# Performance work log

Measured on AMD Instinct MI355X. Metric: run time of the kernel, lower is better.

## Reference

```python
import jax, jax.numpy as jnp
import numpy as np

FEAT_DIM, HIDDEN_DIM, ATTN_DIM = 512, 512, 256
B, N = 32, 4096


def setup_inputs() -> dict:
    key = jax.random.key(0)
    ks = jax.random.split(key, 8)
    s_f = 1.0 / np.sqrt(FEAT_DIM)
    s_h = 1.0 / np.sqrt(HIDDEN_DIM)
    s_a = 1.0 / np.sqrt(ATTN_DIM)
    return {
        "feats": jax.random.normal(ks[0], (B, N, FEAT_DIM), jnp.float32),
        "hidden": jax.random.normal(ks[1], (B, HIDDEN_DIM), jnp.float32),
        "Wf": jax.random.uniform(ks[2], (FEAT_DIM, ATTN_DIM), jnp.float32, -s_f, s_f),
        "bf": jax.random.uniform(ks[3], (ATTN_DIM,), jnp.float32, -s_f, s_f),
        "Wh": jax.random.uniform(ks[4], (HIDDEN_DIM, ATTN_DIM), jnp.float32, -s_h, s_h),
        "bh": jax.random.uniform(ks[5], (ATTN_DIM,), jnp.float32, -s_h, s_h),
        "Ws": jax.random.uniform(ks[6], (ATTN_DIM,), jnp.float32, -s_a, s_a),
        "bs": jax.random.uniform(ks[7], (), jnp.float32, -s_a, s_a),
    }


def reference(feats, hidden, Wf, bf, Wh, bh, Ws, bs):
    # f: (B, N, A); h: (B, 1, A)
    f = jnp.einsum("bnd,da->bna", feats, Wf) + bf
    h = (hidden @ Wh + bh)[:, None, :]
    e = jnp.tanh(f + h)
    scores = jnp.einsum("bna,a->bn", e, Ws) + bs  # (B, N)
    alpha = jax.nn.softmax(scores, axis=1)
    ctx = jnp.einsum("bnd,bn->bd", feats, alpha)  # (B, D)
    return (ctx, alpha)
```

## Files before the change

kernel.cpp:

```cpp
#include <hip/hip_runtime.h>

typedef __attribute__((ext_vector_type(8))) short short8;
typedef __attribute__((ext_vector_type(4))) float f32x4;

#define WFT_OFF 0
#define HB_OFF  262144
#define SC_OFF  294912
#define ST_OFF  819200
#define CP_OFF  835584

#define SMEM_MAIN 76032

__device__ __forceinline__ unsigned short f2bf(float f) {
    unsigned u = __builtin_bit_cast(unsigned, f);
    u += 0x7fffu + ((u >> 16) & 1u);
    return (unsigned short)(u >> 16);
}
__device__ __forceinline__ float bf2f(unsigned short h) {
    unsigned u = ((unsigned)h) << 16;
    return __builtin_bit_cast(float, u);
}
__device__ __forceinline__ float fast_tanh(float x) {
    float e2 = __expf(2.0f * x);
    return 1.0f - 2.0f / (e2 + 1.0f);
}
__device__ __forceinline__ void lds_barrier() {
    asm volatile("s_waitcnt lgkmcnt(0)" ::: "memory");
    __builtin_amdgcn_s_barrier();
}

__global__ void wft_kernel(const float* __restrict__ Wf, unsigned short* __restrict__ WfT) {
    __shared__ unsigned short tl[64 * 80];
    const int t = threadIdx.x;
    const int tk = blockIdx.x >> 2, ta = blockIdx.x & 3;
    const int d0 = tk * 64, a0 = ta * 64;
#pragma unroll
    for (int i = 0; i < 16; ++i) {
        int flat = t + 256 * i;
        int dl = flat >> 6, al = flat & 63;
        tl[al * 80 + dl] = f2bf(Wf[(d0 + dl) * 256 + a0 + al]);
    }
    __syncthreads();
#pragma unroll
    for (int i = 0; i < 2; ++i) {
        int u = t + 256 * i;
        int al = u >> 3, q = u & 7;
        *(uint4*)(&WfT[(size_t)(a0 + al) * 512 + d0 + q * 8]) =
            *(const uint4*)(&tl[al * 80 + q * 8]);
    }
}

__global__ void hb_kernel(const float* __restrict__ hidden, const float* __restrict__ Wh,
                          const float* __restrict__ bh, const float* __restrict__ bfv,
                          float* __restrict__ hb) {
    const int b = blockIdx.x, a = threadIdx.x;
    float acc = bh[a] + bfv[a];
    const float* hrow = hidden + b * 512;
#pragma unroll 8
    for (int d = 0; d < 512; ++d)
        acc += hrow[d] * Wh[d * 256 + a];
    hb[b * 256 + a] = acc;
}

__launch_bounds__(512, 4)
__global__ void main_kernel(const float* __restrict__ feats,
                            const unsigned short* __restrict__ WfT,
                            const float* __restrict__ hbg,
                            const float* __restrict__ Ws,
                            float* __restrict__ scores,
                            float* __restrict__ stats,
                            float* __restrict__ ctxp) {
    extern __shared__ char smem[];
    char* Ab       = smem;
    float* scratch = (float*)(smem + 65536);
    float* wpart   = (float*)(smem + 73728);
    float* wbuf    = (float*)(smem + 75776);

    const int t = threadIdx.x;
    const int tile = blockIdx.x;
    const int b = tile >> 6;
    const int row0 = tile * 64;
    const int lane = t & 63, w = t >> 6;
    const int lr = lane & 15, lg = lane >> 4;
    const int sw = (lr & 7) << 4;

    {
        const int ar = t >> 3;
        const int c8 = t & 7;
        const float4* fr = (const float4*)(feats + (size_t)(row0 + ar) * 512);
        char* arow = Ab + ar * 1024;
        const int rsw = (ar & 7) << 4;
#pragma unroll
        for (int i = 0; i < 16; ++i) {
            int f4 = c8 + i * 8;
            float4 v = fr[f4];
            uint2 u;
            u.x = (unsigned)f2bf(v.x) | ((unsigned)f2bf(v.y) << 16);
            u.y = (unsigned)f2bf(v.z) | ((unsigned)f2bf(v.w) << 16);
            *(uint2*)(arow + ((f4 * 8) ^ rsw)) = u;
        }
    }

    float hbv[2], wsv[2];
#pragma unroll
    for (int j = 0; j < 2; ++j) {
        int col = w * 32 + j * 16 + lr;
        hbv[j] = hbg[b * 256 + col];
        wsv[j] = Ws[col];
    }

    lds_barrier();

    f32x4 acc[4][2] = {};
    const unsigned short* bp0 = WfT + (size_t)(w * 32 + lr) * 512 + lg * 8;
    const unsigned short* bp1 = WfT + (size_t)(w * 32 + 16 + lr) * 512 + lg * 8;

    uint4 bfr[2][2];
    bfr[0][0] = *(const uint4*)(bp0);
    bfr[0][1] = *(const uint4*)(bp1);
#pragma unroll
    for (int ks = 0; ks < 16; ++ks) {
        const int cur = ks & 1, nxt = cur ^ 1;
        if (ks < 15) {
            bfr[nxt][0] = *(const uint4*)(bp0 + (ks + 1) * 32);
            bfr[nxt][1] = *(const uint4*)(bp1 + (ks + 1) * 32);
        }
        short8 af[4];
#pragma unroll
        for (int i = 0; i < 4; ++i) {
            int row = i * 16 + lr;
            af[i] = *(const short8*)(Ab + row * 1024 + ((ks * 64 + lg * 16) ^ sw));
        }
        short8 b0 = __builtin_bit_cast(short8, bfr[cur][0]);
        short8 b1 = __builtin_bit_cast(short8, bfr[cur][1]);
#pragma unroll
        for (int i = 0; i < 4; ++i) {
            acc[i][0] = __builtin_amdgcn_mfma_f32_16x16x32_bf16(af[i], b0, acc[i][0], 0, 0, 0);
            acc[i][1] = __builtin_amdgcn_mfma_f32_16x16x32_bf16(af[i], b1, acc[i][1], 0, 0, 0);
        }
    }

#pragma unroll
    for (int i = 0; i < 4; ++i) {
#pragma unroll
        for (int r = 0; r < 4; ++r) {
            float p = fast_tanh(acc[i][0][r] + hbv[0]) * wsv[0]
                    + fast_tanh(acc[i][1][r] + hbv[1]) * wsv[1];
#pragma unroll
            for (int off = 1; off < 16; off <<= 1) p += __shfl_xor(p, off, 64);
            if (lr == 0) wpart[w * 64 + i * 16 + lg * 4 + r] = p;
        }
    }
    lds_barrier();

    if (t < 64) {
        float s = 0.f;
#pragma unroll
        for (int k = 0; k < 8; ++k) s += wpart[k * 64 + t];
        scores[row0 + t] = s;
        float m = s;
#pragma unroll
        for (int off = 1; off < 64; off <<= 1) m = fmaxf(m, __shfl_xor(m, off, 64));
        float e = __expf(s - m);
        float l = e;
#pragma unroll
        for (int off = 1; off < 64; off <<= 1) l += __shfl_xor(l, off, 64);
        wbuf[t] = e;
        if (t == 0) { stats[tile * 2] = m; stats[tile * 2 + 1] = l; }
    }
    lds_barrier();

    {
        const int nset = t >> 7;
        const int dt = t & 127;
        float accd[4] = {};
#pragma unroll
        for (int nn = 0; nn < 16; ++nn) {
            int n = nset * 16 + nn;
            float wv = wbuf[n];
            unsigned long long a8 =
                *(const unsigned long long*)(Ab + n * 1024 + ((dt * 8) ^ ((n & 7) << 4)));
            accd[0] += wv * bf2f((unsigned short)(a8));
            accd[1] += wv * bf2f((unsigned short)(a8 >> 16));
            accd[2] += wv * bf2f((unsigned short)(a8 >> 32));
            accd[3] += wv * bf2f((unsigned short)(a8 >> 48));
        }
        float4 v;
        v.x = accd[0]; v.y = accd[1]; v.z = accd[2]; v.w = accd[3];
        *(float4*)(scratch + nset * 512 + dt * 4) = v;
    }
    lds_barrier();
    {
        float s = scratch[t] + scratch[512 + t] + scratch[1024 + t] + scratch[1536 + t];
        ctxp[(size_t)tile * 512 + t] = s;
    }
}

__global__ void combine_kernel(const float* __restrict__ scores,
                               const float* __restrict__ stats,
                               const float* __restrict__ ctxp,
                               float* __restrict__ out_ctx,
                               float* __restrict__ out_alpha) {
    __shared__ float scales[64];
    __shared__ float MZ[2];
    const int b = blockIdx.x, t = threadIdx.x;
    if (t < 64) {
        float mk = stats[(b * 64 + t) * 2];
        float lk = stats[(b * 64 + t) * 2 + 1];
        float M = mk;
#pragma unroll
        for (int off = 1; off < 64; off <<= 1) M = fmaxf(M, __shfl_xor(M, off, 64));
        float e = __expf(mk - M);
        float z = lk * e;
#pragma unroll
        for (int off = 1; off < 64; off <<= 1) z += __shfl_xor(z, off, 64);
        scales[t] = e / z;
        if (t == 0) { MZ[0] = M; MZ[1] = z; }
    }
    __syncthreads();
    const float M = MZ[0], invZ = 1.0f / MZ[1];
    const float* sb = scores + b * 4096;
    float* abp = out_alpha + b * 4096;
#pragma unroll
    for (int i = 0; i < 16; ++i) {
        int n = t + 256 * i;
        abp[n] = __expf(sb[n] - M) * invZ;
    }
    const int d0 = t * 2;
    float2 acc; acc.x = 0.f; acc.y = 0.f;
    for (int k = 0; k < 64; ++k) {
        float sc = scales[k];
        const float2 v = *(const float2*)(ctxp + ((size_t)(b * 64 + k) * 512 + d0));
        acc.x += sc * v.x; acc.y += sc * v.y;
    }
    *(float2*)(out_ctx + b * 512 + d0) = acc;
}

extern "C" void kernel_launch(void* const* d_in, const int* in_sizes, int n_in,
                              void* d_out, int out_size, void* d_ws, size_t ws_size,
                              hipStream_t stream) {
    (void)in_sizes; (void)n_in; (void)out_size; (void)ws_size;
    const float* feats  = (const float*)d_in[0];
    const float* hidden = (const float*)d_in[1];
    const float* Wf     = (const float*)d_in[2];
    const float* bfv    = (const float*)d_in[3];
    const float* Wh     = (const float*)d_in[4];
    const float* bh     = (const float*)d_in[5];
    const float* Ws     = (const float*)d_in[6];

    char* ws = (char*)d_ws;
    unsigned short* WfT = (unsigned short*)(ws + WFT_OFF);
    float* hb     = (float*)(ws + HB_OFF);
    float* scores = (float*)(ws + SC_OFF);
    float* stats  = (float*)(ws + ST_OFF);
    float* ctxp   = (float*)(ws + CP_OFF);

    float* out_ctx   = (float*)d_out;
    float* out_alpha = out_ctx + 32 * 512;

    hipFuncSetAttribute((const void*)main_kernel,
                        hipFuncAttributeMaxDynamicSharedMemorySize, SMEM_MAIN);

    hipLaunchKernelGGL(wft_kernel, dim3(32), dim3(256), 0, stream, Wf, WfT);
    hipLaunchKernelGGL(hb_kernel, dim3(32), dim3(256), 0, stream, hidden, Wh, bh, bfv, hb);
    hipLaunchKernelGGL(main_kernel, dim3(2048), dim3(512), SMEM_MAIN, stream,
                       feats, WfT, hb, Ws, scores, stats, ctxp);
    hipLaunchKernelGGL(combine_kernel, dim3(32), dim3(256), 0, stream,
                       scores, stats, ctxp, out_ctx, out_alpha);
}
```

Baseline: 142.0 us.

## Halve main-kernel tile to 32 rows with 256 threads and smaller LDS

```diff
diff --git a/kernel.cpp b/kernel.cpp
--- a/kernel.cpp
+++ b/kernel.cpp
@@ -1,4 +1,5 @@
 #include <hip/hip_runtime.h>
+#include <hip/hip_bf16.h>
 
 typedef __attribute__((ext_vector_type(8))) short short8;
 typedef __attribute__((ext_vector_type(4))) float f32x4;
@@ -7,18 +8,18 @@
 #define HB_OFF  262144
 #define SC_OFF  294912
 #define ST_OFF  819200
-#define CP_OFF  835584
-
-#define SMEM_MAIN 76032
-
-__device__ __forceinline__ unsigned short f2bf(float f) {
-    unsigned u = __builtin_bit_cast(unsigned, f);
-    u += 0x7fffu + ((u >> 16) & 1u);
-    return (unsigned short)(u >> 16);
-}
+#define CP_OFF  851968
+
+#define SMEM_MAIN 33408
+
 __device__ __forceinline__ float bf2f(unsigned short h) {
     unsigned u = ((unsigned)h) << 16;
     return __builtin_bit_cast(float, u);
+}
+__device__ __forceinline__ unsigned pack_bf16(float a, float b) {
+    unsigned short sa = __builtin_bit_cast(unsigned short, __float2bfloat16(a));
+    unsigned short sb = __builtin_bit_cast(unsigned short, __float2bfloat16(b));
+    return (unsigned)sa | ((unsigned)sb << 16);
 }
 __device__ __forceinline__ float fast_tanh(float x) {
     float e2 = __expf(2.0f * x);
@@ -38,7 +39,8 @@
     for (int i = 0; i < 16; ++i) {
         int flat = t + 256 * i;
         int dl = flat >> 6, al = flat & 63;
-        tl[al * 80 + dl] = f2bf(Wf[(d0 + dl) * 256 + a0 + al]);
+        tl[al * 80 + dl] = __builtin_bit_cast(unsigned short,
+                               __float2bfloat16(Wf[(d0 + dl) * 256 + a0 + al]));
     }
     __syncthreads();
 #pragma unroll
@@ -62,7 +64,7 @@
     hb[b * 256 + a] = acc;
 }
 
-__launch_bounds__(512, 4)
+__launch_bounds__(256, 4)
 __global__ void main_kernel(const float* __restrict__ feats,
                             const unsigned short* __restrict__ WfT,
                             const float* __restrict__ hbg,
@@ -71,128 +73,117 @@
                             float* __restrict__ stats,
                             float* __restrict__ ctxp) {
     extern __shared__ char smem[];
-    char* Ab       = smem;
-    float* scratch = (float*)(smem + 65536);
-    float* wpart   = (float*)(smem + 73728);
-    float* wbuf    = (float*)(smem + 75776);
+    char* Ab     = smem;
+    float* wpart = (float*)(smem + 32768);
+    float* wbuf  = (float*)(smem + 33280);
 
     const int t = threadIdx.x;
     const int tile = blockIdx.x;
-    const int b = tile >> 6;
-    const int row0 = tile * 64;
+    const int b = tile >> 7;
+    const int row0 = tile * 32;
     const int lane = t & 63, w = t >> 6;
     const int lr = lane & 15, lg = lane >> 4;
     const int sw = (lr & 7) << 4;
 
     {
-        const int ar = t >> 3;
-        const int c8 = t & 7;
-        const float4* fr = (const float4*)(feats + (size_t)(row0 + ar) * 512);
-        char* arow = Ab + ar * 1024;
-        const int rsw = (ar & 7) << 4;
+        const float4* fp = (const float4*)feats + (size_t)row0 * 128;
+        const int col4 = t & 127;
+        const int r0 = t >> 7;
 #pragma unroll
         for (int i = 0; i < 16; ++i) {
-            int f4 = c8 + i * 8;
-            float4 v = fr[f4];
+            int row = r0 + i * 2;
+            float4 v = fp[(size_t)t + i * 256];
             uint2 u;
-            u.x = (unsigned)f2bf(v.x) | ((unsigned)f2bf(v.y) << 16);
-            u.y = (unsigned)f2bf(v.z) | ((unsigned)f2bf(v.w) << 16);
-            *(uint2*)(arow + ((f4 * 8) ^ rsw)) = u;
-        }
-    }
-
-    float hbv[2], wsv[2];
-#pragma unroll
-    for (int j = 0; j < 2; ++j) {
-        int col = w * 32 + j * 16 + lr;
+            u.x = pack_bf16(v.x, v.y);
+            u.y = pack_bf16(v.z, v.w);
+            *(uint2*)(Ab + row * 1024 + ((col4 * 8) ^ ((row & 7) << 4))) = u;
+        }
+    }
+
+    float hbv[4], wsv[4];
+#pragma unroll
+    for (int j = 0; j < 4; ++j) {
+        int col = w * 64 + j * 16 + lr;
         hbv[j] = hbg[b * 256 + col];
         wsv[j] = Ws[col];
     }
 
     lds_barrier();
 
-    f32x4 acc[4][2] = {};
-    const unsigned short* bp0 = WfT + (size_t)(w * 32 + lr) * 512 + lg * 8;
-    const unsigned short* bp1 = WfT + (size_t)(w * 32 + 16 + lr) * 512 + lg * 8;
-
-    uint4 bfr[2][2];
-    bfr[0][0] = *(const uint4*)(bp0);
-    bfr[0][1] = *(const uint4*)(bp1);
+    f32x4 acc[2][4] = {};
+    const unsigned short* bp[4];
+#pragma unroll
+    for (int j = 0; j < 4; ++j)
+        bp[j] = WfT + (size_t)(w * 64 + j * 16 + lr) * 512 + lg * 8;
+
+    uint4 bfr[2][4];
+#pragma unroll
+    for (int j = 0; j < 4; ++j) bfr[0][j] = *(const uint4*)(bp[j]);
+
 #pragma unroll
     for (int ks = 0; ks < 16; ++ks) {
         const int cur = ks & 1, nxt = cur ^ 1;
         if (ks < 15) {
-            bfr[nxt][0] = *(const uint4*)(bp0 + (ks + 1) * 32);
-            bfr[nxt][1] = *(const uint4*)(bp1 + (ks + 1) * 32);
-        }
-        short8 af[4];
-#pragma unroll
-        for (int i = 0; i < 4; ++i) {
+#pragma unroll
+            for (int j = 0; j < 4; ++j)
+                bfr[nxt][j] = *(const uint4*)(bp[j] + (ks + 1) * 32);
+        }
+        short8 af[2];
+#pragma unroll
+        for (int i = 0; i < 2; ++i) {
             int row = i * 16 + lr;
             af[i] = *(const short8*)(Ab + row * 1024 + ((ks * 64 + lg * 16) ^ sw));
         }
-        short8 b0 = __builtin_bit_cast(short8, bfr[cur][0]);
-        short8 b1 = __builtin_bit_cast(short8, bfr[cur][1]);
-#pragma unroll
-        for (int i = 0; i < 4; ++i) {
-            acc[i][0] = __builtin_amdgcn_mfma_f32_16x16x32_bf16(af[i], b0, acc[i][0], 0, 0, 0);
-            acc[i][1] = __builtin_amdgcn_mfma_f32_16x16x32_bf16(af[i], b1, acc[i][1], 0, 0, 0);
-        }
-    }
-
-#pragma unroll
-    for (int i = 0; i < 4; ++i) {
+#pragma unroll
+        for (int i = 0; i < 2; ++i)
+#pragma unroll
+            for (int j = 0; j < 4; ++j)
+                acc[i][j] = __builtin_amdgcn_mfma_f32_16x16x32_bf16(
+                    af[i], __builtin_bit_cast(short8, bfr[cur][j]), acc[i][j], 0, 0, 0);
+    }
+
+#pragma unroll
+    for (int i = 0; i < 2; ++i) {
 #pragma unroll
         for (int r = 0; r < 4; ++r) {
-            float p = fast_tanh(acc[i][0][r] + hbv[0]) * wsv[0]
-                    + fast_tanh(acc[i][1][r] + hbv[1]) * wsv[1];
+            float p = 0.f;
+#pragma unroll
+            for (int j = 0; j < 4; ++j)
+                p += fast_tanh(acc[i][j][r] + hbv[j]) * wsv[j];
 #pragma unroll
             for (int off = 1; off < 16; off <<= 1) p += __shfl_xor(p, off, 64);
-            if (lr == 0) wpart[w * 64 + i * 16 + lg * 4 + r] = p;
+            if (lr == 0) wpart[w * 32 + i * 16 + lg * 4 + r] = p;
         }
     }
     lds_barrier();
 
-    if (t < 64) {
-        float s = 0.f;
-#pragma unroll
-        for (int k = 0; k < 8; ++k) s += wpart[k * 64 + t];
+    if (t < 32) {
+        float s = wpart[t] + wpart[32 + t] + wpart[64 + t] + wpart[96 + t];
         scores[row0 + t] = s;
         float m = s;
 #pragma unroll
-        for (int off = 1; off < 64; off <<= 1) m = fmaxf(m, __shfl_xor(m, off, 64));
+        for (int off = 1; off < 32; off <<= 1) m = fmaxf(m, __shfl_xor(m, off, 32));
         float e = __expf(s - m);
         float l = e;
 #pragma unroll
-        for (int off = 1; off < 64; off <<= 1) l += __shfl_xor(l, off, 64);
+        for (int off = 1; off < 32; off <<= 1) l += __shfl_xor(l, off, 32);
         wbuf[t] = e;
         if (t == 0) { stats[tile * 2] = m; stats[tile * 2 + 1] = l; }
     }
     lds_barrier();
 
     {
-        const int nset = t >> 7;
-        const int dt = t & 127;
-        float accd[4] = {};
-#pragma unroll
-        for (int nn = 0; nn < 16; ++nn) {
-            int n = nset * 16 + nn;
+        float c0 = 0.f, c1 = 0.f;
+        const int byt = t * 4;
+#pragma unroll 8
+        for (int n = 0; n < 32; ++n) {
             float wv = wbuf[n];
-            unsigned long long a8 =
-                *(const unsigned long long*)(Ab + n * 1024 + ((dt * 8) ^ ((n & 7) << 4)));
-            accd[0] += wv * bf2f((unsigned short)(a8));
-            accd[1] += wv * bf2f((unsigned short)(a8 >> 16));
-            accd[2] += wv * bf2f((unsigned short)(a8 >> 32));
-            accd[3] += wv * bf2f((unsigned short)(a8 >> 48));
-        }
-        float4 v;
-        v.x = accd[0]; v.y = accd[1]; v.z = accd[2]; v.w = accd[3];
-        *(float4*)(scratch + nset * 512 + dt * 4) = v;
-    }
-    lds_barrier();
-    {
-        float s = scratch[t] + scratch[512 + t] + scratch[1024 + t] + scratch[1536 + t];
-        ctxp[(size_t)tile * 512 + t] = s;
+            unsigned a2 = *(const unsigned*)(Ab + n * 1024 + (byt ^ ((n & 7) << 4)));
+            c0 += wv * bf2f((unsigned short)a2);
+            c1 += wv * bf2f((unsigned short)(a2 >> 16));
+        }
+        float2 v; v.x = c0; v.y = c1;
+        *(float2*)(ctxp + (size_t)tile * 512 + t * 2) = v;
     }
 }
 
@@ -201,24 +192,32 @@
                                const float* __restrict__ ctxp,
                                float* __restrict__ out_ctx,
                                float* __restrict__ out_alpha) {
-    __shared__ float scales[64];
-    __shared__ float MZ[2];
+    __shared__ float scales[128];
+    __shared__ float red[4];
     const int b = blockIdx.x, t = threadIdx.x;
-    if (t < 64) {
-        float mk = stats[(b * 64 + t) * 2];
-        float lk = stats[(b * 64 + t) * 2 + 1];
-        float M = mk;
-#pragma unroll
-        for (int off = 1; off < 64; off <<= 1) M = fmaxf(M, __shfl_xor(M, off, 64));
-        float e = __expf(mk - M);
-        float z = lk * e;
-#pragma unroll
-        for (int off = 1; off < 64; off <<= 1) z += __shfl_xor(z, off, 64);
-        scales[t] = e / z;
-        if (t == 0) { MZ[0] = M; MZ[1] = z; }
-    }
-    __syncthreads();
-    const float M = MZ[0], invZ = 1.0f / MZ[1];
+    float mk = -1e30f, lk = 0.f, e = 0.f;
+    if (t < 128) {
+        mk = stats[(b * 128 + t) * 2];
+        lk = stats[(b * 128 + t) * 2 + 1];
+    }
+    float M = mk;
+#pragma unroll
+    for (int off = 1; off < 64; off <<= 1) M = fmaxf(M, __shfl_xor(M, off, 64));
+    if ((t & 63) == 0) red[t >> 6] = M;
+    __syncthreads();
+    M = fmaxf(red[0], red[1]);
+    if (t < 128) e = __expf(mk - M);
+    float z = e * lk;
+#pragma unroll
+    for (int off = 1; off < 64; off <<= 1) z += __shfl_xor(z, off, 64);
+    __syncthreads();
+    if ((t & 63) == 0) red[t >> 6] = z;
+    __syncthreads();
+    const float Z = red[0] + red[1];
+    if (t < 128) scales[t] = e / Z;
+    __syncthreads();
+
+    const float invZ = 1.0f / Z;
     const float* sb = scores + b * 4096;
     float* abp = out_alpha + b * 4096;
 #pragma unroll
@@ -228,9 +227,9 @@
     }
     const int d0 = t * 2;
     float2 acc; acc.x = 0.f; acc.y = 0.f;
-    for (int k = 0; k < 64; ++k) {
+    for (int k = 0; k < 128; ++k) {
         float sc = scales[k];
-        const float2 v = *(const float2*)(ctxp + ((size_t)(b * 64 + k) * 512 + d0));
+        const float2 v = *(const float2*)(ctxp + ((size_t)(b * 128 + k) * 512 + d0));
         acc.x += sc * v.x; acc.y += sc * v.y;
     }
     *(float2*)(out_ctx + b * 512 + d0) = acc;
@@ -263,7 +262,7 @@
 
     hipLaunchKernelGGL(wft_kernel, dim3(32), dim3(256), 0, stream, Wf, WfT);
     hipLaunchKernelGGL(hb_kernel, dim3(32), dim3(256), 0, stream, hidden, Wh, bh, bfv, hb);
-    hipLaunchKernelGGL(main_kernel, dim3(2048), dim3(512), SMEM_MAIN, stream,
+    hipLaunchKernelGGL(main_kernel, dim3(4096), dim3(256), SMEM_MAIN, stream,
                        feats, WfT, hb, Ws, scores, stats, ctxp);
     hipLaunchKernelGGL(combine_kernel, dim3(32), dim3(256), 0, stream,
                        scores, stats, ctxp, out_ctx, out_alpha);
```

Measured after the change: 181.5 us. +27.8%, slower.

## Pre-convert feats to swizzled bf16 image and stream it via async LDS loads

Applied to the files above, without the earlier changes.

```diff
diff --git a/kernel.cpp b/kernel.cpp
--- a/kernel.cpp
+++ b/kernel.cpp
@@ -1,4 +1,5 @@
 #include <hip/hip_runtime.h>
+#include <hip/hip_bf16.h>
 
 typedef __attribute__((ext_vector_type(8))) short short8;
 typedef __attribute__((ext_vector_type(4))) float f32x4;
@@ -8,18 +9,22 @@
 #define SC_OFF  294912
 #define ST_OFF  819200
 #define CP_OFF  835584
-
-#define SMEM_MAIN 76032
-
-__device__ __forceinline__ unsigned short f2bf(float f) {
-    unsigned u = __builtin_bit_cast(unsigned, f);
-    u += 0x7fffu + ((u >> 16) & 1u);
-    return (unsigned short)(u >> 16);
-}
+#define IMG_OFF 8388608
+#define IMG_SZ  134217728
+#define WS_NEED (IMG_OFF + IMG_SZ)
+
+#define SMEM_IMG 149760
+#define SMEM_FB  76032
+
 __device__ __forceinline__ float bf2f(unsigned short h) {
     unsigned u = ((unsigned)h) << 16;
     return __builtin_bit_cast(float, u);
 }
+__device__ __forceinline__ unsigned pack_bf16(float a, float b) {
+    unsigned short sa = __builtin_bit_cast(unsigned short, __float2bfloat16(a));
+    unsigned short sb = __builtin_bit_cast(unsigned short, __float2bfloat16(b));
+    return (unsigned)sa | ((unsigned)sb << 16);
+}
 __device__ __forceinline__ float fast_tanh(float x) {
     float e2 = __expf(2.0f * x);
     return 1.0f - 2.0f / (e2 + 1.0f);
@@ -27,6 +32,11 @@
 __device__ __forceinline__ void lds_barrier() {
     asm volatile("s_waitcnt lgkmcnt(0)" ::: "memory");
     __builtin_amdgcn_s_barrier();
+}
+__device__ __forceinline__ void gld_lds16(const char* g, char* l) {
+    __builtin_amdgcn_global_load_lds(
+        (const __attribute__((address_space(1))) void*)g,
+        (__attribute__((address_space(3))) void*)l, 16, 0, 0);
 }
 
 __global__ void wft_kernel(const float* __restrict__ Wf, unsigned short* __restrict__ WfT) {
@@ -38,7 +48,8 @@
     for (int i = 0; i < 16; ++i) {
         int flat = t + 256 * i;
         int dl = flat >> 6, al = flat & 63;
-        tl[al * 80 + dl] = f2bf(Wf[(d0 + dl) * 256 + a0 + al]);
+        tl[al * 80 + dl] = __builtin_bit_cast(unsigned short,
+                               __float2bfloat16(Wf[(d0 + dl) * 256 + a0 + al]));
     }
     __syncthreads();
 #pragma unroll
@@ -62,14 +73,173 @@
     hb[b * 256 + a] = acc;
 }
 
+__global__ void prep_kernel(const float* __restrict__ feats, char* __restrict__ img) {
+    const int t = threadIdx.x;
+    const size_t tile = blockIdx.x;
+    const char* src = (const char*)feats + tile * 131072;
+    char* dst = img + tile * 65536;
+#pragma unroll
+    for (int i = 0; i < 16; ++i) {
+        int flat = t + 256 * i;
+        int r = flat >> 6, q = flat & 63;
+        const float4* s = (const float4*)(src + r * 2048 + q * 32);
+        float4 v0 = s[0], v1 = s[1];
+        uint4 u;
+        u.x = pack_bf16(v0.x, v0.y); u.y = pack_bf16(v0.z, v0.w);
+        u.z = pack_bf16(v1.x, v1.y); u.w = pack_bf16(v1.z, v1.w);
+        *(uint4*)(dst + r * 1024 + ((q * 16) ^ ((r & 7) << 4))) = u;
+    }
+}
+
+__launch_bounds__(512, 2)
+__global__ void main_img(const char* __restrict__ img,
+                         const unsigned short* __restrict__ WfT,
+                         const float* __restrict__ hbg,
+                         const float* __restrict__ Ws,
+                         float* __restrict__ scores,
+                         float* __restrict__ stats,
+                         float* __restrict__ ctxp) {
+    extern __shared__ char smem[];
+    float* wpart   = (float*)(smem + 131072);
+    float* wbuf    = (float*)(smem + 133120);
+    float* scratch = (float*)(smem + 133376);
+
+    const int t = threadIdx.x, bid = blockIdx.x;
+    const int lane = t & 63, w = t >> 6;
+    const int lr = lane & 15, lg = lane >> 4;
+    const int sw = (lr & 7) << 4;
+    const int b = bid >> 3;
+
+    float hbv[2], wsv[2];
+#pragma unroll
+    for (int j = 0; j < 2; ++j) {
+        int col = w * 32 + j * 16 + lr;
+        hbv[j] = hbg[b * 256 + col];
+        wsv[j] = Ws[col];
+    }
+
+    {
+        const char* src = img + (size_t)(bid * 8) * 65536 + w * 8192 + lane * 16;
+        char* dst = smem + w * 8192;
+#pragma unroll
+        for (int i = 0; i < 8; ++i) gld_lds16(src + i * 1024, dst + i * 1024);
+    }
+
+    for (int it = 0; it < 8; ++it) {
+        const int tile = bid * 8 + it;
+        const int row0 = tile * 64;
+        char* Ab = smem + ((it & 1) << 16);
+
+        if (it < 7) {
+            const char* src = img + (size_t)(tile + 1) * 65536 + w * 8192 + lane * 16;
+            char* dst = smem + (((it + 1) & 1) << 16) + w * 8192;
+#pragma unroll
+            for (int i = 0; i < 8; ++i) gld_lds16(src + i * 1024, dst + i * 1024);
+            asm volatile("s_waitcnt vmcnt(8)" ::: "memory");
+        } else {
+            asm volatile("s_waitcnt vmcnt(0)" ::: "memory");
+        }
+        __builtin_amdgcn_s_barrier();
+
+        const unsigned short* bp0 = WfT + (size_t)(w * 32 + lr) * 512 + lg * 8;
+        const unsigned short* bp1 = WfT + (size_t)(w * 32 + 16 + lr) * 512 + lg * 8;
+        uint4 bq[2][2];
+        bq[0][0] = *(const uint4*)(bp0);
+        bq[0][1] = *(const uint4*)(bp1);
+        bq[1][0] = *(const uint4*)(bp0 + 32);
+        bq[1][1] = *(const uint4*)(bp1 + 32);
+
+        f32x4 acc[4][2] = {};
+#pragma unroll
+        for (int ks = 0; ks < 16; ++ks) {
+            const int p = ks & 1;
+            short8 af[4];
+#pragma unroll
+            for (int i = 0; i < 4; ++i) {
+                int row = i * 16 + lr;
+                af[i] = *(const short8*)(Ab + row * 1024 + ((ks * 64 + lg * 16) ^ sw));
+            }
+            short8 b0 = __builtin_bit_cast(short8, bq[p][0]);
+            short8 b1 = __builtin_bit_cast(short8, bq[p][1]);
+            if (ks < 14) {
+                bq[p][0] = *(const uint4*)(bp0 + (ks + 2) * 32);
+                bq[p][1] = *(const uint4*)(bp1 + (ks + 2) * 32);
+            }
+#pragma unroll
+            for (int i = 0; i < 4; ++i) {
+                acc[i][0] = __builtin_amdgcn_mfma_f32_16x16x32_bf16(af[i], b0, acc[i][0], 0, 0, 0);
+                acc[i][1] = __builtin_amdgcn_mfma_f32_16x16x32_bf16(af[i], b1, acc[i][1], 0, 0, 0);
+            }
+        }
+
+#pragma unroll
+        for (int i = 0; i < 4; ++i) {
+#pragma unroll
+            for (int r = 0; r < 4; ++r) {
+                float p = fast_tanh(acc[i][0][r] + hbv[0]) * wsv[0]
+                        + fast_tanh(acc[i][1][r] + hbv[1]) * wsv[1];
+#pragma unroll
+                for (int off = 1; off < 16; off <<= 1) p += __shfl_xor(p, off, 64);
+                if (lr == 0) wpart[w * 64 + i * 16 + lg * 4 + r] = p;
+            }
+        }
+        lds_barrier();
+
+        if (t < 64) {
+            float s = 0.f;
+#pragma unroll
+            for (int k = 0; k < 8; ++k) s += wpart[k * 64 + t];
+            scores[row0 + t] = s;
+            float m = s;
+#pragma unroll
+            for (int off = 1; off < 64; off <<= 1) m = fmaxf(m, __shfl_xor(m, off, 64));
+            float e = __expf(s - m);
+            float l = e;
+#pragma unroll
+            for (int off = 1; off < 64; off <<= 1) l += __shfl_xor(l, off, 64);
+            wbuf[t] = e;
+            if (t == 0) { stats[tile * 2] = m; stats[tile * 2 + 1] = l; }
+        }
+        lds_barrier();
+
+        {
+            float accd[8] = {};
+            const int nset = t >> 6, dg = t & 63;
+            const int d0 = dg * 8;
+#pragma unroll
+            for (int nn = 0; nn < 8; ++nn) {
+                int n = nset * 8 + nn;
+                float wv = wbuf[n];
+                short8 av = *(const short8*)(Ab + n * 1024 + ((d0 * 2) ^ ((n & 7) << 4)));
+#pragma unroll
+                for (int e = 0; e < 8; ++e)
+                    accd[e] += wv * bf2f((unsigned short)av[e]);
+            }
+            float4 v0, v1;
+            v0.x = accd[0]; v0.y = accd[1]; v0.z = accd[2]; v0.w = accd[3];
+            v1.x = accd[4]; v1.y = accd[5]; v1.z = accd[6]; v1.w = accd[7];
+            *(float4*)(scratch + nset * 512 + d0) = v0;
+            *(float4*)(scratch + nset * 512 + d0 + 4) = v1;
+        }
+        lds_barrier();
+        {
+            float s = 0.f;
+#pragma unroll
+            for (int ns = 0; ns < 8; ++ns) s += scratch[ns * 512 + t];
+            ctxp[(size_t)tile * 512 + t] = s;
+        }
+        lds_barrier();
+    }
+}
+
 __launch_bounds__(512, 4)
-__global__ void main_kernel(const float* __restrict__ feats,
-                            const unsigned short* __restrict__ WfT,
-                            const float* __restrict__ hbg,
-                            const float* __restrict__ Ws,
-                            float* __restrict__ scores,
-                            float* __restrict__ stats,
-                            float* __restrict__ ctxp) {
+__global__ void main_fb(const float* __restrict__ feats,
+                        const unsigned short* __restrict__ WfT,
+                        const float* __restrict__ hbg,
+                        const float* __restrict__ Ws,
+                        float* __restrict__ scores,
+                        float* __restrict__ stats,
+                        float* __restrict__ ctxp) {
     extern __shared__ char smem[];
     char* Ab       = smem;
     float* scratch = (float*)(smem + 65536);
@@ -95,8 +265,8 @@
             int f4 = c8 + i * 8;
             float4 v = fr[f4];
             uint2 u;
-            u.x = (unsigned)f2bf(v.x) | ((unsigned)f2bf(v.y) << 16);
-            u.y = (unsigned)f2bf(v.z) | ((unsigned)f2bf(v.w) << 16);
+            u.x = pack_bf16(v.x, v.y);
+            u.y = pack_bf16(v.z, v.w);
             *(uint2*)(arow + ((f4 * 8) ^ rsw)) = u;
         }
     }
@@ -227,19 +397,26 @@
         abp[n] = __expf(sb[n] - M) * invZ;
     }
     const int d0 = t * 2;
-    float2 acc; acc.x = 0.f; acc.y = 0.f;
-    for (int k = 0; k < 64; ++k) {
-        float sc = scales[k];
-        const float2 v = *(const float2*)(ctxp + ((size_t)(b * 64 + k) * 512 + d0));
-        acc.x += sc * v.x; acc.y += sc * v.y;
-    }
-    *(float2*)(out_ctx + b * 512 + d0) = acc;
+    const float* cb = ctxp + (size_t)b * 64 * 512;
+    float accx = 0.f, accy = 0.f;
+    for (int k0 = 0; k0 < 64; k0 += 8) {
+        float2 v[8]; float s[8];
+#pragma unroll
+        for (int u = 0; u < 8; ++u) {
+            s[u] = scales[k0 + u];
+            v[u] = *(const float2*)(cb + (size_t)(k0 + u) * 512 + d0);
+        }
+#pragma unroll
+        for (int u = 0; u < 8; ++u) { accx += s[u] * v[u].x; accy += s[u] * v[u].y; }
+    }
+    float2 o; o.x = accx; o.y = accy;
+    *(float2*)(out_ctx + b * 512 + d0) = o;
 }
 
 extern "C" void kernel_launch(void* const* d_in, const int* in_sizes, int n_in,
                               void* d_out, int out_size, void* d_ws, size_t ws_size,
                               hipStream_t stream) {
-    (void)in_sizes; (void)n_in; (void)out_size; (void)ws_size;
+    (void)in_sizes; (void)n_in; (void)out_size;
     const float* feats  = (const float*)d_in[0];
     const float* hidden = (const float*)d_in[1];
     const float* Wf     = (const float*)d_in[2];
@@ -254,17 +431,27 @@
     float* scores = (float*)(ws + SC_OFF);
     float* stats  = (float*)(ws + ST_OFF);
     float* ctxp   = (float*)(ws + CP_OFF);
+    char*  img    = ws + IMG_OFF;
 
     float* out_ctx   = (float*)d_out;
     float* out_alpha = out_ctx + 32 * 512;
 
-    hipFuncSetAttribute((const void*)main_kernel,
-                        hipFuncAttributeMaxDynamicSharedMemorySize, SMEM_MAIN);
+    hipFuncSetAttribute((const void*)main_img,
+                        hipFuncAttributeMaxDynamicSharedMemorySize, SMEM_IMG);
+    hipFuncSetAttribute((const void*)main_fb,
+                        hipFuncAttributeMaxDynamicSharedMemorySize, SMEM_FB);
 
     hipLaunchKernelGGL(wft_kernel, dim3(32), dim3(256), 0, stream, Wf, WfT);
     hipLaunchKernelGGL(hb_kernel, dim3(32), dim3(256), 0, stream, hidden, Wh, bh, bfv, hb);
-    hipLaunchKernelGGL(main_kernel, dim3(2048), dim3(512), SMEM_MAIN, stream,
-                       feats, WfT, hb, Ws, scores, stats, ctxp);
+
+    if (ws_size >= (size_t)WS_NEED) {
+        hipLaunchKernelGGL(prep_kernel, dim3(2048), dim3(256), 0, stream, feats, img);
+        hipLaunchKernelGGL(main_img, dim3(256), dim3(512), SMEM_IMG, stream,
+                           img, WfT, hb, Ws, scores, stats, ctxp);
+    } else {
+        hipLaunchKernelGGL(main_fb, dim3(2048), dim3(512), SMEM_FB, stream,
+                           feats, WfT, hb, Ws, scores, stats, ctxp);
+    }
     hipLaunchKernelGGL(combine_kernel, dim3(32), dim3(256), 0, stream,
                        scores, stats, ctxp, out_ctx, out_alpha);
 }
```

Result: slower. 227.5 us (+60.3%).

## Split context accumulation out of the scores kernel into a separate fp32 pass

Applied to the files above, without the earlier changes.

```diff
diff --git a/kernel.cpp b/kernel.cpp
--- a/kernel.cpp
+++ b/kernel.cpp
@@ -1,4 +1,5 @@
 #include <hip/hip_runtime.h>
+#include <hip/hip_bf16.h>
 
 typedef __attribute__((ext_vector_type(8))) short short8;
 typedef __attribute__((ext_vector_type(4))) float f32x4;
@@ -9,16 +10,16 @@
 #define ST_OFF  819200
 #define CP_OFF  835584
 
-#define SMEM_MAIN 76032
-
-__device__ __forceinline__ unsigned short f2bf(float f) {
-    unsigned u = __builtin_bit_cast(unsigned, f);
-    u += 0x7fffu + ((u >> 16) & 1u);
-    return (unsigned short)(u >> 16);
-}
+#define SMEM_S 67584
+
 __device__ __forceinline__ float bf2f(unsigned short h) {
     unsigned u = ((unsigned)h) << 16;
     return __builtin_bit_cast(float, u);
+}
+__device__ __forceinline__ unsigned pack_bf16(float a, float b) {
+    unsigned short sa = __builtin_bit_cast(unsigned short, __float2bfloat16(a));
+    unsigned short sb = __builtin_bit_cast(unsigned short, __float2bfloat16(b));
+    return (unsigned)sa | ((unsigned)sb << 16);
 }
 __device__ __forceinline__ float fast_tanh(float x) {
     float e2 = __expf(2.0f * x);
@@ -38,7 +39,8 @@
     for (int i = 0; i < 16; ++i) {
         int flat = t + 256 * i;
         int dl = flat >> 6, al = flat & 63;
-        tl[al * 80 + dl] = f2bf(Wf[(d0 + dl) * 256 + a0 + al]);
+        tl[al * 80 + dl] = __builtin_bit_cast(unsigned short,
+                               __float2bfloat16(Wf[(d0 + dl) * 256 + a0 + al]));
     }
     __syncthreads();
 #pragma unroll
@@ -63,18 +65,15 @@
 }
 
 __launch_bounds__(512, 4)
-__global__ void main_kernel(const float* __restrict__ feats,
-                            const unsigned short* __restrict__ WfT,
-                            const float* __restrict__ hbg,
-                            const float* __restrict__ Ws,
-                            float* __restrict__ scores,
-                            float* __restrict__ stats,
-                            float* __restrict__ ctxp) {
+__global__ void scores_kernel(const float* __restrict__ feats,
+                              const unsigned short* __restrict__ WfT,
+                              const float* __restrict__ hbg,
+                              const float* __restrict__ Ws,
+                              float* __restrict__ scores,
+                              float* __restrict__ stats) {
     extern __shared__ char smem[];
-    char* Ab       = smem;
-    float* scratch = (float*)(smem + 65536);
-    float* wpart   = (float*)(smem + 73728);
-    float* wbuf    = (float*)(smem + 75776);
+    char* Ab     = smem;
+    float* wpart = (float*)(smem + 65536);
 
     const int t = threadIdx.x;
     const int tile = blockIdx.x;
@@ -95,8 +94,8 @@
             int f4 = c8 + i * 8;
             float4 v = fr[f4];
             uint2 u;
-            u.x = (unsigned)f2bf(v.x) | ((unsigned)f2bf(v.y) << 16);
-            u.y = (unsigned)f2bf(v.z) | ((unsigned)f2bf(v.w) << 16);
+            u.x = pack_bf16(v.x, v.y);
+            u.y = pack_bf16(v.z, v.w);
             *(uint2*)(arow + ((f4 * 8) ^ rsw)) = u;
         }
     }
@@ -111,28 +110,30 @@
 
     lds_barrier();
 
-    f32x4 acc[4][2] = {};
     const unsigned short* bp0 = WfT + (size_t)(w * 32 + lr) * 512 + lg * 8;
     const unsigned short* bp1 = WfT + (size_t)(w * 32 + 16 + lr) * 512 + lg * 8;
-
-    uint4 bfr[2][2];
-    bfr[0][0] = *(const uint4*)(bp0);
-    bfr[0][1] = *(const uint4*)(bp1);
+    uint4 bq[2][2];
+    bq[0][0] = *(const uint4*)(bp0);
+    bq[0][1] = *(const uint4*)(bp1);
+    bq[1][0] = *(const uint4*)(bp0 + 32);
+    bq[1][1] = *(const uint4*)(bp1 + 32);
+
+    f32x4 acc[4][2] = {};
 #pragma unroll
     for (int ks = 0; ks < 16; ++ks) {
-        const int cur = ks & 1, nxt = cur ^ 1;
-        if (ks < 15) {
-            bfr[nxt][0] = *(const uint4*)(bp0 + (ks + 1) * 32);
-            bfr[nxt][1] = *(const uint4*)(bp1 + (ks + 1) * 32);
-        }
+        const int p = ks & 1;
         short8 af[4];
 #pragma unroll
         for (int i = 0; i < 4; ++i) {
             int row = i * 16 + lr;
             af[i] = *(const short8*)(Ab + row * 1024 + ((ks * 64 + lg * 16) ^ sw));
         }
-        short8 b0 = __builtin_bit_cast(short8, bfr[cur][0]);
-        short8 b1 = __builtin_bit_cast(short8, bfr[cur][1]);
+        short8 b0 = __builtin_bit_cast(short8, bq[p][0]);
+        short8 b1 = __builtin_bit_cast(short8, bq[p][1]);
+        if (ks < 14) {
+            bq[p][0] = *(const uint4*)(bp0 + (ks + 2) * 32);
+            bq[p][1] = *(const uint4*)(bp1 + (ks + 2) * 32);
+        }
 #pragma unroll
         for (int i = 0; i < 4; ++i) {
             acc[i][0] = __builtin_amdgcn_mfma_f32_16x16x32_bf16(af[i], b0, acc[i][0], 0, 0, 0);
@@ -165,35 +166,37 @@
         float l = e;
 #pragma unroll
         for (int off = 1; off < 64; off <<= 1) l += __shfl_xor(l, off, 64);
-        wbuf[t] = e;
         if (t == 0) { stats[tile * 2] = m; stats[tile * 2 + 1] = l; }
     }
-    lds_barrier();
-
-    {
-        const int nset = t >> 7;
-        const int dt = t & 127;
-        float accd[4] = {};
-#pragma unroll
-        for (int nn = 0; nn < 16; ++nn) {
-            int n = nset * 16 + nn;
-            float wv = wbuf[n];
-            unsigned long long a8 =
-                *(const unsigned long long*)(Ab + n * 1024 + ((dt * 8) ^ ((n & 7) << 4)));
-            accd[0] += wv * bf2f((unsigned short)(a8));
-            accd[1] += wv * bf2f((unsigned short)(a8 >> 16));
-            accd[2] += wv * bf2f((unsigned short)(a8 >> 32));
-            accd[3] += wv * bf2f((unsigned short)(a8 >> 48));
-        }
-        float4 v;
-        v.x = accd[0]; v.y = accd[1]; v.z = accd[2]; v.w = accd[3];
-        *(float4*)(scratch + nset * 512 + dt * 4) = v;
-    }
-    lds_barrier();
-    {
-        float s = scratch[t] + scratch[512 + t] + scratch[1024 + t] + scratch[1536 + t];
-        ctxp[(size_t)tile * 512 + t] = s;
-    }
+}
+
+__launch_bounds__(256, 8)
+__global__ void ctx_kernel(const float* __restrict__ feats,
+                           const float* __restrict__ scores,
+                           const float* __restrict__ stats,
+                           float* __restrict__ ctxp) {
+    __shared__ float wbuf[64];
+    const int tile = blockIdx.x;
+    const int row0 = tile * 64;
+    const int t = threadIdx.x;
+
+    if (t < 64) wbuf[t] = __expf(scores[row0 + t] - stats[tile * 2]);
+    __syncthreads();
+
+    const float* fb = feats + (size_t)row0 * 512 + t * 2;
+    float accx = 0.f, accy = 0.f;
+    for (int n0 = 0; n0 < 64; n0 += 8) {
+        float2 v[8]; float sc[8];
+#pragma unroll
+        for (int u = 0; u < 8; ++u) {
+            sc[u] = wbuf[n0 + u];
+            v[u]  = *(const float2*)(fb + (size_t)(n0 + u) * 512);
+        }
+#pragma unroll
+        for (int u = 0; u < 8; ++u) { accx += sc[u] * v[u].x; accy += sc[u] * v[u].y; }
+    }
+    float2 o; o.x = accx; o.y = accy;
+    *(float2*)(ctxp + (size_t)tile * 512 + t * 2) = o;
 }
 
 __global__ void combine_kernel(const float* __restrict__ scores,
@@ -227,13 +230,20 @@
         abp[n] = __expf(sb[n] - M) * invZ;
     }
     const int d0 = t * 2;
-    float2 acc; acc.x = 0.f; acc.y = 0.f;
-    for (int k = 0; k < 64; ++k) {
-        float sc = scales[k];
-        const float2 v = *(const float2*)(ctxp + ((size_t)(b * 64 + k) * 512 + d0));
-        acc.x += sc * v.x; acc.y += sc * v.y;
-    }
-    *(float2*)(out_ctx + b * 512 + d0) = acc;
+    const float* cb = ctxp + (size_t)b * 64 * 512;
+    float accx = 0.f, accy = 0.f;
+    for (int k0 = 0; k0 < 64; k0 += 8) {
+        float2 v[8]; float s[8];
+#pragma unroll
+        for (int u = 0; u < 8; ++u) {
+            s[u] = scales[k0 + u];
+            v[u] = *(const float2*)(cb + (size_t)(k0 + u) * 512 + d0);
+        }
+#pragma unroll
+        for (int u = 0; u < 8; ++u) { accx += s[u] * v[u].x; accy += s[u] * v[u].y; }
+    }
+    float2 o; o.x = accx; o.y = accy;
+    *(float2*)(out_ctx + b * 512 + d0) = o;
 }
 
 extern "C" void kernel_launch(void* const* d_in, const int* in_sizes, int n_in,
@@ -258,13 +268,15 @@
     float* out_ctx   = (float*)d_out;
     float* out_alpha = out_ctx + 32 * 512;
 
-    hipFuncSetAttribute((const void*)main_kernel,
-                        hipFuncAttributeMaxDynamicSharedMemorySize, SMEM_MAIN);
+    hipFuncSetAttribute((const void*)scores_kernel,
+                        hipFuncAttributeMaxDynamicSharedMemorySize, SMEM_S);
 
     hipLaunchKernelGGL(wft_kernel, dim3(32), dim3(256), 0, stream, Wf, WfT);
     hipLaunchKernelGGL(hb_kernel, dim3(32), dim3(256), 0, stream, hidden, Wh, bh, bfv, hb);
-    hipLaunchKernelGGL(main_kernel, dim3(2048), dim3(512), SMEM_MAIN, stream,
-                       feats, WfT, hb, Ws, scores, stats, ctxp);
+    hipLaunchKernelGGL(scores_kernel, dim3(2048), dim3(512), SMEM_S, stream,
+                       feats, WfT, hb, Ws, scores, stats);
+    hipLaunchKernelGGL(ctx_kernel, dim3(2048), dim3(256), 0, stream,
+                       feats, scores, stats, ctxp);
     hipLaunchKernelGGL(combine_kernel, dim3(32), dim3(256), 0, stream,
                        scores, stats, ctxp, out_ctx, out_alpha);
 }
```

Measured after the change: 184.7 us. 30.1% more time.
